# Optimization experiments

Hardware: AMD Instinct MI355X
Metric: run time of the kernel (lower is better)

Reference implementation:

```python
import jax, jax.numpy as jnp
import numpy as np

NUM_GRAPHS = 1024
NODES_PER_GRAPH = 9
EDGES_PER_GRAPH = NODES_PER_GRAPH * (NODES_PER_GRAPH - 1)  # 72, fully connected no self-loops
N = NUM_GRAPHS * NODES_PER_GRAPH
E = NUM_GRAPHS * EDGES_PER_GRAPH
POS_DIM = 64
HID = 256          # gnn_hidden_dim / common_gnn_dim
S1_FEAT = HID      # stage1 feature_dim (after projection)
S1_INT = S1_FEAT + POS_DIM           # 320
S2_FEAT = 2 * HID                    # 512 (two scales concatenated)
S2_OUT = 2 * HID                     # 512
S2_INT = S2_FEAT + POS_DIM           # 576
LN_EPS = 1e-5
SM_EPS = 1e-16  # PyG softmax eps


def _dense(x, w, b):
    return x @ w + b


def _layer_norm(x, g, b):
    mu = jnp.mean(x, axis=-1, keepdims=True)
    var = jnp.mean(jnp.square(x - mu), axis=-1, keepdims=True)
    return (x - mu) * jax.lax.rsqrt(var + LN_EPS) * g + b


def _segment_softmax(logits, idx, n):
    # logits: [E,1]; normalize over edges sharing the same destination node
    m = jax.ops.segment_max(logits, idx, num_segments=n)
    e = jnp.exp(logits - m[idx])
    s = jax.ops.segment_sum(e, idx, num_segments=n)
    return e / (s[idx] + SM_EPS)


def _gnn_layer(x, pos, src, dst, n, p):
    # x: [N, F], pos: [N, P]; edges src->dst (PyG: edge_index[0]=src j, edge_index[1]=dst i)
    ix = jnp.concatenate([x, pos], axis=-1)            # integrated_x [N, F+P]
    ii, ij = ix[dst], ix[src]                          # integrated_x_i / _j per edge
    # pairwise_fn(integrated_x_j, integrated_x_i) -> mlp(cat([integrated_x_i, integrated_x_j]))
    pw_in = jnp.concatenate([ii, ij], axis=-1)         # [E, 2*(F+P)]
    rel = _dense(jax.nn.gelu(_dense(pw_in, p['pw1_w'], p['pw1_b']), approximate=False),
                 p['pw2_w'], p['pw2_b'])               # [E, out]
    att_in = jnp.concatenate([x[dst], x[src], pos[dst], pos[src]], axis=-1)
    logits = _dense(jax.nn.leaky_relu(_dense(att_in, p['att1_w'], p['att1_b']), 0.01),
                    p['att2_w'], p['att2_b'])          # [E, 1]
    attw = _segment_softmax(logits, dst, n)
    aggr = jax.ops.segment_sum(attw * rel, dst, num_segments=n)  # [N, out]
    upd = jax.nn.gelu(_dense(jnp.concatenate([ix, aggr], axis=-1), p['upd_w'], p['upd_b']),
                      approximate=False)
    h = _dense(ix, p['skip_w'], p['skip_b']) + upd
    return _layer_norm(h, p['ln_g'], p['ln_b'])


def _glorot(key, shape):
    fan_in, fan_out = shape[0], shape[1]
    lim = np.sqrt(6.0 / (fan_in + fan_out))
    return jax.random.uniform(key, shape, jnp.float32, -lim, lim)


def setup_inputs() -> dict:
    key = jax.random.key(0)
    ks = iter(jax.random.split(key, 64))

    feat_low = jax.random.normal(next(ks), (N, 512), jnp.float32)
    feat_high = jax.random.normal(next(ks), (N, 1024), jnp.float32)
    batch_indices = jnp.repeat(jnp.arange(NUM_GRAPHS), NODES_PER_GRAPH).astype(jnp.int32)

    # fully connected (no self loop) edges within each 9-node graph
    loc = np.array([(j, i) for i in range(NODES_PER_GRAPH) for j in range(NODES_PER_GRAPH) if i != j],
                   dtype=np.int64)  # (src, dst)
    off = np.repeat(np.arange(NUM_GRAPHS) * NODES_PER_GRAPH, EDGES_PER_GRAPH)
    src = np.tile(loc[:, 0], NUM_GRAPHS) + off
    dst = np.tile(loc[:, 1], NUM_GRAPHS) + off
    edge_index = jnp.asarray(np.stack([src, dst]), dtype=jnp.int32)  # [2, E]

    inp = dict(feat_low=feat_low, feat_high=feat_high,
               batch_indices=batch_indices, edge_index=edge_index)

    inp['pos_table'] = jax.random.normal(next(ks), (NODES_PER_GRAPH, POS_DIM), jnp.float32)
    inp['proj_low_w'] = _glorot(next(ks), (512, HID)); inp['proj_low_b'] = jnp.zeros((HID,), jnp.float32)
    inp['proj_high_w'] = _glorot(next(ks), (1024, HID)); inp['proj_high_b'] = jnp.zeros((HID,), jnp.float32)

    def layer_params(pref, fdim, pdim, out):
        integ = fdim + pdim
        d = {}
        d[pref + 'pw1_w'] = _glorot(next(ks), (2 * integ, out)); d[pref + 'pw1_b'] = jnp.zeros((out,), jnp.float32)
        d[pref + 'pw2_w'] = _glorot(next(ks), (out, out)); d[pref + 'pw2_b'] = jnp.zeros((out,), jnp.float32)
        d[pref + 'att1_w'] = _glorot(next(ks), (2 * fdim + 2 * pdim, out)); d[pref + 'att1_b'] = jnp.zeros((out,), jnp.float32)
        d[pref + 'att2_w'] = _glorot(next(ks), (out, 1)); d[pref + 'att2_b'] = jnp.zeros((1,), jnp.float32)
        d[pref + 'upd_w'] = _glorot(next(ks), (integ + out, out)); d[pref + 'upd_b'] = jnp.zeros((out,), jnp.float32)
        d[pref + 'ln_g'] = jnp.ones((out,), jnp.float32); d[pref + 'ln_b'] = jnp.zeros((out,), jnp.float32)
        d[pref + 'skip_w'] = _glorot(next(ks), (integ, out)); d[pref + 'skip_b'] = jnp.zeros((out,), jnp.float32)
        return d

    inp.update(layer_params('s1_', S1_FEAT, POS_DIM, HID))
    inp.update(layer_params('s2_', S2_FEAT, POS_DIM, S2_OUT))

    inp['cls1_w'] = _glorot(next(ks), (S2_OUT, HID)); inp['cls1_b'] = jnp.zeros((HID,), jnp.float32)
    inp['cls2_w'] = _glorot(next(ks), (HID, 1)); inp['cls2_b'] = jnp.zeros((1,), jnp.float32)
    return inp


def _forward(feat_low, feat_high, pos_table,
             proj_low_w, proj_low_b, proj_high_w, proj_high_b,
             s1, s2, cls1_w, cls1_b, cls2_w, cls2_b,
             batch_indices, edge_index):
    src, dst = edge_index[0], edge_index[1]
    pos_ids = jnp.tile(jnp.arange(NODES_PER_GRAPH), NUM_GRAPHS)
    pos = pos_table[pos_ids]                                  # [N, P]
    h_low = _gnn_layer(_dense(feat_low, proj_low_w, proj_low_b), pos, src, dst, N, s1)
    h_high = _gnn_layer(_dense(feat_high, proj_high_w, proj_high_b), pos, src, dst, N, s1)
    unified = jnp.concatenate([h_low, h_high], axis=-1)       # [N, 512]
    h2 = _gnn_layer(unified, pos, src, dst, N, s2)            # [N, 512]
    pooled = jax.ops.segment_sum(h2, batch_indices, num_segments=NUM_GRAPHS)
    hid = jax.nn.gelu(_dense(pooled, cls1_w, cls1_b), approximate=False)
    return _dense(hid, cls2_w, cls2_b)                        # [G, 1]


S1_KEYS = ['pw1_w', 'pw1_b', 'pw2_w', 'pw2_b', 'att1_w', 'att1_b', 'att2_w', 'att2_b',
           'upd_w', 'upd_b', 'ln_g', 'ln_b', 'skip_w', 'skip_b']


def reference(feat_low, feat_high, batch_indices, edge_index, pos_table,
              proj_low_w, proj_low_b, proj_high_w, proj_high_b,
              s1_pw1_w, s1_pw1_b, s1_pw2_w, s1_pw2_b, s1_att1_w, s1_att1_b,
              s1_att2_w, s1_att2_b, s1_upd_w, s1_upd_b, s1_ln_g, s1_ln_b,
              s1_skip_w, s1_skip_b,
              s2_pw1_w, s2_pw1_b, s2_pw2_w, s2_pw2_b, s2_att1_w, s2_att1_b,
              s2_att2_w, s2_att2_b, s2_upd_w, s2_upd_b, s2_ln_g, s2_ln_b,
              s2_skip_w, s2_skip_b,
              cls1_w, cls1_b, cls2_w, cls2_b):
    s1 = dict(zip(S1_KEYS, [s1_pw1_w, s1_pw1_b, s1_pw2_w, s1_pw2_b, s1_att1_w, s1_att1_b,
                            s1_att2_w, s1_att2_b, s1_upd_w, s1_upd_b, s1_ln_g, s1_ln_b,
                            s1_skip_w, s1_skip_b]))
    s2 = dict(zip(S1_KEYS, [s2_pw1_w, s2_pw1_b, s2_pw2_w, s2_pw2_b, s2_att1_w, s2_att1_b,
                            s2_att2_w, s2_att2_b, s2_upd_w, s2_upd_b, s2_ln_g, s2_ln_b,
                            s2_skip_w, s2_skip_b]))
    return _forward(feat_low, feat_high, pos_table,
                    proj_low_w, proj_low_b, proj_high_w, proj_high_b,
                    s1, s2, cls1_w, cls1_b, cls2_w, cls2_b,
                    batch_indices, edge_index)
```

## Files before the change

### kernel.cpp

```cpp
#include <hip/hip_runtime.h>
#include <math.h>

#define NUM_GRAPHS 1024
#define NPG 9
#define NN 9216
#define NN2 18432
#define POSD 64

typedef __attribute__((ext_vector_type(8))) short bf16x8;
typedef __attribute__((ext_vector_type(4))) float f32x4;

__device__ __forceinline__ float gelu_f(float x) {
    return 0.5f * x * (1.0f + erff(x * 0.70710678118654752f));
}
__device__ __forceinline__ float gelu_fast(float x) {
    float y = 0.7978845608f * x * (1.0f + 0.044715f * x * x);
    float t = __expf(-2.0f * fabsf(y));
    float r = (1.0f - t) / (1.0f + t);
    r = copysignf(r, y);
    return 0.5f * x * (1.0f + r);
}
__device__ __forceinline__ ushort f2b(float v) {
    unsigned u = __float_as_uint(v);
    return (ushort)((u + 0x7fffu + ((u >> 16) & 1u)) >> 16);
}
__device__ __forceinline__ float b2f(ushort u) {
    return __uint_as_float(((unsigned)u) << 16);
}
__device__ __forceinline__ void gload16(const ushort* g, ushort* l) {
    __builtin_amdgcn_global_load_lds((const __attribute__((address_space(1))) void*)g,
                                     (__attribute__((address_space(3))) void*)l, 16, 0, 0);
}

__global__ __launch_bounds__(256, 3) void mgemm(
    const ushort* __restrict__ A, int lda,
    const ushort* __restrict__ Wt, int ldw,
    const float* __restrict__ bias1,
    const float* __restrict__ prow, int ldp,
    float* outF, ushort* outB, int ldo,
    long partStride, int K)
{
    __shared__ ushort sA[3][128 * 32];
    __shared__ ushort sB[3][128 * 32];
    const int wv = threadIdx.x >> 6, lane = threadIdx.x & 63;
    const int rh = wv & 1, ch = wv >> 1;

    const int GX = gridDim.x;
    const int nwg = GX * gridDim.y;
    const int flat = blockIdx.y * GX + blockIdx.x;
    const int swq = nwg >> 3, swr = nwg & 7;
    const int xcd = flat & 7, posi = flat >> 3;
    const int tix = (xcd < swr ? xcd * (swq + 1) : swr * (swq + 1) + (xcd - swr) * swq) + posi;
    const int m0 = (tix / GX) * 128, n0 = (tix % GX) * 128;

    const int koff = blockIdx.z * K;

    f32x4 acc[4][4];
#pragma unroll
    for (int i = 0; i < 4; i++)
#pragma unroll
        for (int j = 0; j < 4; j++) acc[i][j] = (f32x4){0.f, 0.f, 0.f, 0.f};

    const ushort* Ab = A + (size_t)m0 * lda + koff;
    const ushort* Wb = Wt + (size_t)n0 * ldw + koff;
    if (outF) outF += (size_t)blockIdx.z * partStride;

    auto stage = [&](int b, int k0) {
#pragma unroll
        for (int i = 0; i < 2; i++) {
            int c = wv * 2 + i;
            int u = c * 64 + lane;
            int row = u >> 2, p = u & 3;
            int q = (p - (row >> 1)) & 3;
            gload16(Ab + (size_t)row * lda + k0 + q * 8, sA[b] + c * 512);
            gload16(Wb + (size_t)row * ldw + k0 + q * 8, sB[b] + c * 512);
        }
    };

    const int nsteps = K >> 5;
    stage(0, 0);
    stage(1, 32);
    int cur = 0;
    for (int s = 0; s < nsteps; s++) {
        if (s + 1 < nsteps) {
            asm volatile("s_waitcnt vmcnt(4)" ::: "memory");
        } else {
            asm volatile("s_waitcnt vmcnt(0)" ::: "memory");
        }
        __builtin_amdgcn_s_barrier();
        __builtin_amdgcn_sched_barrier(0);
        if (s + 2 < nsteps) {
            int nb = cur + 2; if (nb >= 3) nb -= 3;
            stage(nb, (s + 2) << 5);
        }

        const int qg = lane >> 4;
        bf16x8 af[4], bfr[4];
#pragma unroll
        for (int bi = 0; bi < 4; bi++) {
            int r = rh * 64 + bi * 16 + (lane & 15);
            af[bi] = *(const bf16x8*)(sA[cur] + (r * 4 + ((qg + (r >> 1)) & 3)) * 8);
        }
#pragma unroll
        for (int bj = 0; bj < 4; bj++) {
            int r = ch * 64 + bj * 16 + (lane & 15);
            bfr[bj] = *(const bf16x8*)(sB[cur] + (r * 4 + ((qg + (r >> 1)) & 3)) * 8);
        }
        __builtin_amdgcn_s_setprio(1);
#pragma unroll
        for (int bi = 0; bi < 4; bi++)
#pragma unroll
            for (int bj = 0; bj < 4; bj++)
                acc[bi][bj] = __builtin_amdgcn_mfma_f32_16x16x32_bf16(
                    af[bi], bfr[bj], acc[bi][bj], 0, 0, 0);
        __builtin_amdgcn_s_setprio(0);
        __builtin_amdgcn_sched_barrier(0);
        cur++; if (cur >= 3) cur -= 3;
    }

    float* sP = (float*)sA;
    const bool haveP = (prow != 0);
    if (haveP) {
        __syncthreads();
        for (int i = threadIdx.x; i < 9 * 128; i += 256) {
            int rr = i >> 7, c = i & 127;
            sP[rr * 129 + c] = prow[(size_t)rr * ldp + n0 + c] + bias1[n0 + c];
        }
        __syncthreads();
    }

#pragma unroll
    for (int bi = 0; bi < 4; bi++) {
#pragma unroll
        for (int r = 0; r < 4; r++) {
            int m = m0 + rh * 64 + bi * 16 + (lane >> 4) * 4 + r;
            int r9 = m % 9;
#pragma unroll
            for (int bj = 0; bj < 4; bj++) {
                int nc = ch * 64 + bj * 16 + (lane & 15);
                int n = n0 + nc;
                float v = acc[bi][bj][r];
                if (haveP) v += sP[r9 * 129 + nc];
                if (outF) outF[(size_t)m * ldo + n] = v;
                if (outB) outB[(size_t)m * ldo + n] = f2b(v);
            }
        }
    }
}

struct PJArg {
    const ushort* A[2];
    const ushort* W[2];
    const float*  bias[2];
    ushort*       out[2];
    int lda[2], K[2];
};

__global__ __launch_bounds__(256, 3) void pjgemm(PJArg pa)
{
    __shared__ ushort sA[3][128 * 32];
    __shared__ ushort sB[3][128 * 32];
    const int z = blockIdx.z;
    const ushort* __restrict__ A  = pa.A[z];
    const ushort* __restrict__ Wt = pa.W[z];
    const float*  __restrict__ bias = pa.bias[z];
    ushort* out = pa.out[z];
    const int lda = pa.lda[z], ldw = lda, K = pa.K[z];

    const int wv = threadIdx.x >> 6, lane = threadIdx.x & 63;
    const int rh = wv & 1, ch = wv >> 1;

    const int GX = gridDim.x;
    const int nwg = GX * gridDim.y;
    const int flat = blockIdx.y * GX + blockIdx.x;
    const int swq = nwg >> 3, swr = nwg & 7;
    const int xcd = flat & 7, posi = flat >> 3;
    const int tix = (xcd < swr ? xcd * (swq + 1) : swr * (swq + 1) + (xcd - swr) * swq) + posi;
    const int m0 = (tix / GX) * 128, n0 = (tix % GX) * 128;

    f32x4 acc[4][4];
#pragma unroll
    for (int i = 0; i < 4; i++)
#pragma unroll
        for (int j = 0; j < 4; j++) acc[i][j] = (f32x4){0.f, 0.f, 0.f, 0.f};

    const ushort* Ab = A + (size_t)m0 * lda;
    const ushort* Wb = Wt + (size_t)n0 * ldw;

    auto stage = [&](int b, int k0) {
#pragma unroll
        for (int i = 0; i < 2; i++) {
            int c = wv * 2 + i;
            int u = c * 64 + lane;
            int row = u >> 2, p = u & 3;
            int q = (p - (row >> 1)) & 3;
            gload16(Ab + (size_t)row * lda + k0 + q * 8, sA[b] + c * 512);
            gload16(Wb + (size_t)row * ldw + k0 + q * 8, sB[b] + c * 512);
        }
    };

    const int nsteps = K >> 5;
    stage(0, 0);
    stage(1, 32);
    int cur = 0;
    for (int s = 0; s < nsteps; s++) {
        if (s + 1 < nsteps) {
            asm volatile("s_waitcnt vmcnt(4)" ::: "memory");
        } else {
            asm volatile("s_waitcnt vmcnt(0)" ::: "memory");
        }
        __builtin_amdgcn_s_barrier();
        __builtin_amdgcn_sched_barrier(0);
        if (s + 2 < nsteps) {
            int nb = cur + 2; if (nb >= 3) nb -= 3;
            stage(nb, (s + 2) << 5);
        }

        const int qg = lane >> 4;
        bf16x8 af[4], bfr[4];
#pragma unroll
        for (int bi = 0; bi < 4; bi++) {
            int r = rh * 64 + bi * 16 + (lane & 15);
            af[bi] = *(const bf16x8*)(sA[cur] + (r * 4 + ((qg + (r >> 1)) & 3)) * 8);
        }
#pragma unroll
        for (int bj = 0; bj < 4; bj++) {
            int r = ch * 64 + bj * 16 + (lane & 15);
            bfr[bj] = *(const bf16x8*)(sB[cur] + (r * 4 + ((qg + (r >> 1)) & 3)) * 8);
        }
        __builtin_amdgcn_s_setprio(1);
#pragma unroll
        for (int bi = 0; bi < 4; bi++)
#pragma unroll
            for (int bj = 0; bj < 4; bj++)
                acc[bi][bj] = __builtin_amdgcn_mfma_f32_16x16x32_bf16(
                    af[bi], bfr[bj], acc[bi][bj], 0, 0, 0);
        __builtin_amdgcn_s_setprio(0);
        __builtin_amdgcn_sched_barrier(0);
        cur++; if (cur >= 3) cur -= 3;
    }

    float* sBias = (float*)sA;
    __syncthreads();
    if (threadIdx.x < 128) sBias[threadIdx.x] = bias[n0 + threadIdx.x];
    __syncthreads();

#pragma unroll
    for (int bi = 0; bi < 4; bi++) {
#pragma unroll
        for (int r = 0; r < 4; r++) {
            int m = m0 + rh * 64 + bi * 16 + (lane >> 4) * 4 + r;
#pragma unroll
            for (int bj = 0; bj < 4; bj++) {
                int nc = ch * 64 + bj * 16 + (lane & 15);
                float v = acc[bi][bj][r] + sBias[nc];
                out[(size_t)m * 512 + n0 + nc] = f2b(v);
            }
        }
    }
}

#define NJOBS 16
struct TJobsArg {
    const float* src[NJOBS];
    long dst[NJOBS];
    int K[NJOBS], N[NJOBS], off0[NJOBS], ldo[NJOBS];
};

__global__ __launch_bounds__(256) void tw_kernel(TJobsArg ja, ushort* wbuf)
{
    int j = blockIdx.y;
    int K = ja.K[j], N = ja.N[j];
    int tk = K >> 5, tn = N >> 5;
    int t = blockIdx.x;
    if (t >= tk * tn) return;
    int kt = t % tk, nt = t / tk;
    const float* src = ja.src[j];
    ushort* out = wbuf + ja.dst[j];
    int ldo = ja.ldo[j];
    __shared__ float L[32][33];
    int r = threadIdx.x >> 5, c = threadIdx.x & 31;
#pragma unroll
    for (int rr = 0; rr < 4; rr++) {
        int k = kt * 32 + rr * 8 + r;
        L[rr * 8 + r][c] = src[(size_t)(ja.off0[j] + k) * N + nt * 32 + c];
    }
    __syncthreads();
#pragma unroll
    for (int rr = 0; rr < 4; rr++) {
        int n = nt * 32 + rr * 8 + r;
        out[(size_t)n * ldo + kt * 32 + c] = f2b(L[c][rr * 8 + r]);
    }
}

__global__ __launch_bounds__(256) void edge_kernel(
    const ushort* __restrict__ PB, const float* __restrict__ att2_w,
    ushort* __restrict__ Gout, int ldG, float* __restrict__ S, int O, int cshift)
{
    __shared__ ushort sPB[9 * 1024];
    __shared__ float sAw[512];
    __shared__ float logits[72];
    __shared__ float aw[72];
    const int g = blockIdx.x;
    const int tid = threadIdx.x, lane = tid & 63, wave = tid >> 6;
    const int O2 = O * 2, O5 = O * 5;
    const int tpr = O >> 8;
    const int tcount = 9 * tpr;
    const ushort* gbase = PB + (size_t)g * 9 * O5;

    for (int i = wave; i < tcount; i += 4) {
        int row = i / tpr, co = i - row * tpr;
        gload16(gbase + (size_t)row * O5 + O2 + co * 512 + lane * 8, sPB + i * 512);
    }
    for (int c = tid; c < O; c += 256) sAw[c] = att2_w[c];
    __syncthreads();

    for (int e = wave; e < 72; e += 4) {
        int d = e >> 3, k = e & 7;
        int s = k + (k >= d);
        const ushort* ad = sPB + d * O2;
        const ushort* as = sPB + s * O2 + O;
        float p = 0.f;
        for (int c0 = lane * 4; c0 < O; c0 += 256) {
            ushort4 a4 = *(const ushort4*)(ad + c0);
            ushort4 s4 = *(const ushort4*)(as + c0);
            const ushort* ap = (const ushort*)&a4;
            const ushort* sp = (const ushort*)&s4;
#pragma unroll
            for (int j = 0; j < 4; j++) {
                float v = b2f(ap[j]) + b2f(sp[j]);
                v = v > 0.f ? v : 0.01f * v;
                p += v * sAw[c0 + j];
            }
        }
#pragma unroll
        for (int off = 32; off; off >>= 1) p += __shfl_down(p, off, 64);
        if (lane == 0) logits[e] = p;
    }
    __syncthreads();

    for (int i = wave; i < tcount; i += 4) {
        int row = i / tpr, co = i - row * tpr;
        gload16(gbase + (size_t)row * O5 + co * 512 + lane * 8, sPB + i * 512);
    }

    if (tid < 9) {
        float m = -INFINITY;
#pragma unroll
        for (int k = 0; k < 8; k++) m = fmaxf(m, logits[tid * 8 + k]);
        float s = 0.f, ee[8];
#pragma unroll
        for (int k = 0; k < 8; k++) { ee[k] = expf(logits[tid * 8 + k] - m); s += ee[k]; }
        float inv = 1.0f / (s + 1e-16f);
#pragma unroll
        for (int k = 0; k < 8; k++) aw[tid * 8 + k] = ee[k] * inv;
        S[g * 9 + tid] = s * inv;
    }
    __syncthreads();

    const int nch = O >> 3;
    for (int idx = tid; idx < 9 * nch; idx += 256) {
        int n = idx >> cshift, cc = idx & (nch - 1);
        bf16x8 pdv = *(const bf16x8*)(sPB + n * O2 + cc * 8);
        const ushort* pp = (const ushort*)&pdv;
        float pdf[8];
#pragma unroll
        for (int j = 0; j < 8; j++) pdf[j] = b2f(pp[j]);
        float acc8[8];
#pragma unroll
        for (int j = 0; j < 8; j++) acc8[j] = 0.f;
#pragma unroll
        for (int k = 0; k < 8; k++) {
            int s = k + (k >= n);
            float w = aw[n * 8 + k];
            bf16x8 psv = *(const bf16x8*)(sPB + s * O2 + O + cc * 8);
            const ushort* qp = (const ushort*)&psv;
#pragma unroll
            for (int j = 0; j < 8; j++)
                acc8[j] += w * gelu_fast(pdf[j] + b2f(qp[j]));
        }
        ushort o8[8];
#pragma unroll
        for (int j = 0; j < 8; j++) o8[j] = f2b(acc8[j]);
        *(bf16x8*)(Gout + (size_t)(g * 9 + n) * ldG + cc * 8) = *(const bf16x8*)o8;
    }
}

__global__ __launch_bounds__(256) void ln_kernel(
    const float* __restrict__ P0, const float* __restrict__ P1,
    const float* __restrict__ ub, const float* __restrict__ vb,
    const float* __restrict__ S, const float* __restrict__ posU,
    const ushort* __restrict__ PBs, int ld5,
    const float* __restrict__ gw, const float* __restrict__ bw,
    ushort* outB, int ldoB, int rowsplit, float* outF, int O)
{
    __shared__ float sm[4];
    const int n = blockIdx.x, tid = threadIdx.x;
    const int lane = tid & 63, wid = tid >> 6;
    const float* p0 = P0 + (size_t)n * O;
    const float* p1 = P1 ? P1 + (size_t)n * O : 0;
    const ushort* sr = PBs + (size_t)n * ld5;
    const float* pu = posU + (size_t)(n % 9) * O;
    const float sv = S[n];
    const int cnt = O >> 8;

    float vals[2];
    float sum = 0.f;
#pragma unroll
    for (int i = 0; i < 2; i++) {
        if (i < cnt) {
            int c = tid + 256 * i;
            float t = p0[c] + (p1 ? p1[c] : 0.f) + ub[c] + vb[c] * sv + pu[c];
            vals[i] = gelu_f(t) + b2f(sr[c]);
            sum += vals[i];
        }
    }
#pragma unroll
    for (int off = 32; off; off >>= 1) sum += __shfl_down(sum, off, 64);
    if (lane == 0) sm[wid] = sum;
    __syncthreads();
    const float mu = (sm[0] + sm[1] + sm[2] + sm[3]) / (float)O;
    __syncthreads();

    float var = 0.f;
#pragma unroll
    for (int i = 0; i < 2; i++) {
        if (i < cnt) { float d = vals[i] - mu; var += d * d; }
    }
#pragma unroll
    for (int off = 32; off; off >>= 1) var += __shfl_down(var, off, 64);
    if (lane == 0) sm[wid] = var;
    __syncthreads();
    const float rstd = rsqrtf((sm[0] + sm[1] + sm[2] + sm[3]) / (float)O + 1e-5f);

    int orow = n, coloff = 0;
    if (n >= rowsplit) { orow = n - rowsplit; coloff = 256; }
#pragma unroll
    for (int i = 0; i < 2; i++) {
        if (i < cnt) {
            int c = tid + 256 * i;
            float v = (vals[i] - mu) * rstd * gw[c] + bw[c];
            if (outB) outB[(size_t)orow * ldoB + coloff + c] = f2b(v);
            if (outF) outF[(size_t)n * O + c] = v;
        }
    }
}

__global__ void prep_kernel(
    const float* __restrict__ pw1_b1, const float* __restrict__ att1_b1, const float* __restrict__ skip_b1,
    const float* __restrict__ pw1_b2, const float* __restrict__ att1_b2, const float* __restrict__ skip_b2,
    const float* __restrict__ pos_table,
    const float* __restrict__ s1_pw1, const float* __restrict__ s1_att, const float* __restrict__ s1_skp,
    const float* __restrict__ s2_pw1, const float* __restrict__ s2_att, const float* __restrict__ s2_skp,
    const float* __restrict__ pw2_b1, const float* __restrict__ upd_w1,
    const float* __restrict__ pw2_b2, const float* __restrict__ upd_w2,
    const float* __restrict__ pw2_w1, const float* __restrict__ pw2_w2,
    const float* __restrict__ feat_low, const float* __restrict__ feat_high,
    float* biasC1, float* biasC2,
    float* posPB1, float* posPB2, float* posU1, float* posU2,
    float* vb1, float* vb2, ushort* pw2f1, ushort* pw2f2, ushort* featB)
{
    int i = blockIdx.x * 256 + threadIdx.x;
    if (i < 1280) {
        float v;
        if (i < 256) v = pw1_b1[i];
        else if (i < 512) v = 0.f;
        else if (i < 768) v = att1_b1[i - 512];
        else if (i < 1024) v = 0.f;
        else v = skip_b1[i - 1024];
        biasC1[i] = v;
        return;
    }
    i -= 1280;
    if (i < 2560) {
        float v;
        if (i < 512) v = pw1_b2[i];
        else if (i < 1024) v = 0.f;
        else if (i < 1536) v = att1_b2[i - 1024];
        else if (i < 2048) v = 0.f;
        else v = skip_b2[i - 2048];
        biasC2[i] = v;
        return;
    }
    i -= 2560;
    if (i < 9 * 1280) {
        int r = i / 1280, n = i - r * 1280;
        int sec = n >> 8, c = n & 255;
        const float* src; int row0;
        if (sec == 0) { src = s1_pw1; row0 = 256; }
        else if (sec == 1) { src = s1_pw1; row0 = 576; }
        else if (sec == 2) { src = s1_att; row0 = 512; }
        else if (sec == 3) { src = s1_att; row0 = 576; }
        else { src = s1_skp; row0 = 256; }
        float a = 0.f;
        for (int k = 0; k < 64; k++) a += pos_table[r * 64 + k] * src[(size_t)(row0 + k) * 256 + c];
        posPB1[i] = a;
        return;
    }
    i -= 9 * 1280;
    if (i < 9 * 2560) {
        int r = i / 2560, n = i - r * 2560;
        int sec = n >> 9, c = n & 511;
        const float* src; int row0;
        if (sec == 0) { src = s2_pw1; row0 = 512; }
        else if (sec == 1) { src = s2_pw1; row0 = 1088; }
        else if (sec == 2) { src = s2_att; row0 = 1024; }
        else if (sec == 3) { src = s2_att; row0 = 1088; }
        else { src = s2_skp; row0 = 512; }
        float a = 0.f;
        for (int k = 0; k < 64; k++) a += pos_table[r * 64 + k] * src[(size_t)(row0 + k) * 512 + c];
        posPB2[i] = a;
        return;
    }
    i -= 9 * 2560;
    if (i < 9 * 256) {
        int r = i >> 8, c = i & 255;
        float a = 0.f;
        for (int k = 0; k < 64; k++) a += pos_table[r * 64 + k] * upd_w1[(size_t)(256 + k) * 256 + c];
        posU1[i] = a;
        return;
    }
    i -= 9 * 256;
    if (i < 9 * 512) {
        int r = i >> 9, c = i & 511;
        float a = 0.f;
        for (int k = 0; k < 64; k++) a += pos_table[r * 64 + k] * upd_w2[(size_t)(512 + k) * 512 + c];
        posU2[i] = a;
        return;
    }
    i -= 9 * 512;
    if (i < 256) {
        float a = 0.f;
        for (int j = 0; j < 256; j++) a += pw2_b1[j] * upd_w1[(size_t)(320 + j) * 256 + i];
        vb1[i] = a;
        return;
    }
    i -= 256;
    if (i < 512) {
        float a = 0.f;
        for (int j = 0; j < 512; j++) a += pw2_b2[j] * upd_w2[(size_t)(576 + j) * 512 + i];
        vb2[i] = a;
        return;
    }
    i -= 512;
    if (i < 256 * 256) { pw2f1[i] = f2b(pw2_w1[i]); return; }
    i -= 256 * 256;
    if (i < 512 * 512) { pw2f2[i] = f2b(pw2_w2[i]); return; }
    i -= 512 * 512;
    if (i < NN * 512 / 4) {
        float4 v = ((const float4*)feat_low)[i];
        ushort4 o;
        o.x = f2b(v.x); o.y = f2b(v.y); o.z = f2b(v.z); o.w = f2b(v.w);
        ((ushort4*)featB)[i] = o;
        return;
    }
    i -= NN * 512 / 4;
    if (i < NN * 1024 / 4) {
        float4 v = ((const float4*)feat_high)[i];
        ushort4 o;
        o.x = f2b(v.x); o.y = f2b(v.y); o.z = f2b(v.z); o.w = f2b(v.w);
        ((ushort4*)(featB + (size_t)NN * 512))[i] = o;
    }
}

__global__ __launch_bounds__(256) void head_kernel(
    const float* __restrict__ h2,
    const float* __restrict__ cls1_w, const float* __restrict__ cls1_b,
    const float* __restrict__ cls2_w, const float* __restrict__ cls2_b,
    float* __restrict__ out)
{
    __shared__ float pooled[4][512];
    __shared__ float hid[4][256];
    const int b = blockIdx.x, tid = threadIdx.x;

    for (int idx = tid; idx < 4 * 512; idx += 256) {
        int gi = idx >> 9, c = idx & 511;
        const float* base = h2 + (size_t)((b * 4 + gi) * 9) * 512 + c;
        float s = 0.f;
#pragma unroll
        for (int k = 0; k < NPG; k++) s += base[(size_t)k * 512];
        pooled[gi][c] = s;
    }
    __syncthreads();

    {
        float acc[4] = {0.f, 0.f, 0.f, 0.f};
        for (int c = 0; c < 512; c++) {
            float w = cls1_w[(size_t)c * 256 + tid];
#pragma unroll
            for (int gi = 0; gi < 4; gi++) acc[gi] += pooled[gi][c] * w;
        }
        float bb = cls1_b[tid];
#pragma unroll
        for (int gi = 0; gi < 4; gi++) hid[gi][tid] = gelu_f(acc[gi] + bb);
    }
    __syncthreads();

    {
        int gi = tid >> 6, lane = tid & 63;
        float p = 0.f;
#pragma unroll
        for (int i = 0; i < 4; i++) p += hid[gi][lane + 64 * i] * cls2_w[lane + 64 * i];
#pragma unroll
        for (int off = 32; off; off >>= 1) p += __shfl_down(p, off, 64);
        if (lane == 0) out[b * 4 + gi] = p + cls2_b[0];
    }
}

static inline void mg(hipStream_t st, int M, int N, int K,
                      const ushort* A, int lda, const ushort* Wt, int ldw,
                      const float* bias1, const float* prow, int ldp,
                      float* outF, ushort* outB, int ldo,
                      int nz, long partStride)
{
    dim3 grid(N / 128, M / 128, nz);
    mgemm<<<grid, dim3(256), 0, st>>>(A, lda, Wt, ldw, bias1, prow, ldp,
                                      outF, outB, ldo, partStride, K);
}

extern "C" void kernel_launch(void* const* d_in, const int* in_sizes, int n_in,
                              void* d_out, int out_size, void* d_ws, size_t ws_size,
                              hipStream_t stream)
{
    (void)in_sizes; (void)n_in; (void)out_size; (void)ws_size;
    const float* feat_low   = (const float*)d_in[0];
    const float* feat_high  = (const float*)d_in[1];
    const float* pos_table  = (const float*)d_in[4];
    const float* proj_low_w  = (const float*)d_in[5];
    const float* proj_low_b  = (const float*)d_in[6];
    const float* proj_high_w = (const float*)d_in[7];
    const float* proj_high_b = (const float*)d_in[8];
    const float* cls1_w = (const float*)d_in[37];
    const float* cls1_b = (const float*)d_in[38];
    const float* cls2_w = (const float*)d_in[39];
    const float* cls2_b = (const float*)d_in[40];
    float* out = (float*)d_out;

    const float* s1_pw1 = (const float*)d_in[9];
    const float* s1_att = (const float*)d_in[13];
    const float* s1_upd = (const float*)d_in[17];
    const float* s1_skp = (const float*)d_in[21];
    const float* s2_pw1 = (const float*)d_in[23];
    const float* s2_att = (const float*)d_in[27];
    const float* s2_upd = (const float*)d_in[31];
    const float* s2_skp = (const float*)d_in[35];

    const float* att2_w1 = (const float*)d_in[15];
    const float* upd_b1  = (const float*)d_in[18];
    const float* ln_g1   = (const float*)d_in[19];
    const float* ln_b1   = (const float*)d_in[20];
    const float* att2_w2 = (const float*)d_in[29];
    const float* upd_b2  = (const float*)d_in[32];
    const float* ln_g2   = (const float*)d_in[33];
    const float* ln_b2   = (const float*)d_in[34];

    char* base = (char*)d_ws;
    size_t cur = 0;
    auto alloc = [&](size_t bytes) { void* p = base + cur; cur += (bytes + 255) & ~(size_t)255; return p; };
    void*   PBreg = alloc((size_t)NN * 2560 * 2);
    ushort* PB    = (ushort*)PBreg;
    ushort* featB = (ushort*)PBreg;
    void*   IX1reg = alloc((size_t)NN2 * 512 * 2);
    ushort* ixa1  = (ushort*)IX1reg;
    float*  h2    = (float*)IX1reg;
    ushort* ixa2  = (ushort*)alloc((size_t)NN * 1024 * 2);
    float*  PT    = (float*)alloc((size_t)4 * NN * 256 * 4);
    float*  S     = (float*)alloc((size_t)NN2 * 4);
    float*  biasC1 = (float*)alloc(1280 * 4);
    float*  biasC2 = (float*)alloc(2560 * 4);
    float*  posPB1 = (float*)alloc(9 * 1280 * 4);
    float*  posPB2 = (float*)alloc(9 * 2560 * 4);
    float*  posU1  = (float*)alloc(9 * 256 * 4);
    float*  posU2  = (float*)alloc(9 * 512 * 4);
    float*  vb1   = (float*)alloc(256 * 4);
    float*  vb2   = (float*)alloc(512 * 4);
    ushort* wbuf  = (ushort*)alloc((size_t)3400000 * 2);

    TJobsArg ja;
    long woff[16];
    {
        struct J { const float* s; int K, N, off0, ldo; long sz; };
        J js[NJOBS] = {
            {proj_low_w,  512, 256, 0, 512, 512L * 256},
            {proj_high_w, 1024, 256, 0, 1024, 1024L * 256},
            {s1_pw1, 256, 256, 0, 256, 256L * 256},
            {s1_pw1, 256, 256, 320, 256, 256L * 256},
            {s1_att, 256, 256, 0, 256, 256L * 256},
            {s1_att, 256, 256, 256, 256, 256L * 256},
            {s1_skp, 256, 256, 0, 256, 256L * 256},
            {s1_upd, 256, 256, 0, 512, 512L * 256},
            {s1_upd, 256, 256, 320, 256, 256L * 256},
            {s2_pw1, 512, 512, 0, 512, 512L * 512},
            {s2_pw1, 512, 512, 576, 512, 512L * 512},
            {s2_att, 512, 512, 0, 512, 512L * 512},
            {s2_att, 512, 512, 512, 512, 512L * 512},
            {s2_skp, 512, 512, 0, 512, 512L * 512},
            {s2_upd, 512, 512, 0, 1024, 1024L * 512},
            {s2_upd, 512, 512, 576, 512, 512L * 512},
        };
        long off = 0;
        for (int i = 0; i < NJOBS; i++) {
            ja.src[i] = js[i].s; ja.K[i] = js[i].K; ja.N[i] = js[i].N;
            ja.off0[i] = js[i].off0; ja.ldo[i] = js[i].ldo;
            ja.dst[i] = off; woff[i] = off;
            off += js[i].sz;
        }
    }
    long pw2off1 = woff[15] + 512L * 512;
    long pw2off2 = pw2off1 + 256L * 256;
    tw_kernel<<<dim3(256, NJOBS), dim3(256), 0, stream>>>(ja, wbuf);

    ushort* wBig5_1 = wbuf + woff[2];
    ushort* updW1   = wbuf + woff[7];
    ushort* updbT1  = wbuf + woff[8];
    ushort* wBig5_2 = wbuf + woff[9];
    ushort* updW2   = wbuf + woff[14];
    ushort* updbT2  = wbuf + woff[15];
    ushort* pw2f1   = wbuf + pw2off1;
    ushort* pw2f2   = wbuf + pw2off2;

    {
        long tot = 1280 + 2560 + 9 * 1280 + 9 * 2560 + 9 * 256 + 9 * 512
                 + 256 + 512 + 256 * 256 + 512 * 512
                 + (long)NN * 512 / 4 + (long)NN * 1024 / 4;
        prep_kernel<<<dim3((unsigned)((tot + 255) / 256)), dim3(256), 0, stream>>>(
            (const float*)d_in[10], (const float*)d_in[14], (const float*)d_in[22],
            (const float*)d_in[24], (const float*)d_in[28], (const float*)d_in[36],
            pos_table,
            s1_pw1, s1_att, s1_skp, s2_pw1, s2_att, s2_skp,
            (const float*)d_in[12], s1_upd, (const float*)d_in[26], s2_upd,
            (const float*)d_in[11], (const float*)d_in[25],
            feat_low, feat_high,
            biasC1, biasC2, posPB1, posPB2, posU1, posU2, vb1, vb2, pw2f1, pw2f2, featB);
    }

    mg(stream, 256, 256, 256, updbT1, 256, pw2f1, 256, 0, 0, 0, 0, updW1 + 256, 512, 1, 0);
    mg(stream, 512, 512, 512, updbT2, 512, pw2f2, 512, 0, 0, 0, 0, updW2 + 512, 1024, 1, 0);

    {
        PJArg pa;
        pa.A[0] = featB;                      pa.lda[0] = 512;  pa.K[0] = 512;
        pa.A[1] = featB + (size_t)NN * 512;   pa.lda[1] = 1024; pa.K[1] = 1024;
        pa.W[0] = wbuf + woff[0];
        pa.W[1] = wbuf + woff[1];
        pa.bias[0] = proj_low_b;
        pa.bias[1] = proj_high_b;
        pa.out[0] = ixa1;
        pa.out[1] = ixa1 + (size_t)NN * 512;
        pjgemm<<<dim3(2, NN / 128, 2), dim3(256), 0, stream>>>(pa);
    }

    mg(stream, NN2, 1280, 256, ixa1, 512, wBig5_1, 256, biasC1, posPB1, 1280, 0, PB, 1280, 1, 0);
    edge_kernel<<<dim3(2 * NUM_GRAPHS), dim3(256), 0, stream>>>(
        PB, att2_w1, ixa1 + 256, 512, S, 256, 5);
    mg(stream, NN2, 256, 512, ixa1, 512, updW1, 512, 0, 0, 0, PT, 0, 256, 1, 0);
    ln_kernel<<<dim3(NN2), dim3(256), 0, stream>>>(
        PT, 0, upd_b1, vb1, S, posU1,
        PB + 4 * 256, 1280, ln_g1, ln_b1, ixa2, 1024, NN, 0, 256);

    mg(stream, NN, 2560, 512, ixa2, 1024, wBig5_2, 512, biasC2, posPB2, 2560, 0, PB, 2560, 1, 0);
    edge_kernel<<<dim3(NUM_GRAPHS), dim3(256), 0, stream>>>(
        PB, att2_w2, ixa2 + 512, 1024, S, 512, 6);
    mg(stream, NN, 512, 1024, ixa2, 1024, updW2, 1024, 0, 0, 0, PT, 0, 512, 1, 0);
    ln_kernel<<<dim3(NN), dim3(256), 0, stream>>>(
        PT, 0, upd_b2, vb2, S, posU2,
        PB + 4 * 512, 2560, ln_g2, ln_b2, 0, 0, 1 << 30, h2, 512);

    head_kernel<<<dim3(NUM_GRAPHS / 4), dim3(256), 0, stream>>>(h2, cls1_w, cls1_b, cls2_w, cls2_b, out);
}
```

Before: 552.5 us.

## Stage GEMM epilogue through LDS, write bf16 update outputs, one-wave-per-row LayerNorm

The GEMM epilogue now packs bf16 results into a padded LDS tile and writes full rows with 16-byte stores, where it used to do scattered per-element global stores. The fp32 output path is removed. The update GEMMs now emit bf16 into a smaller PT buffer, which halves the traffic they write and the LayerNorm then reads. The LayerNorm kernel is reworked so each wave handles one row with vector loads and xor-shuffle reductions, with no shared memory or block barriers. This trades some precision in the pre-activation values for less memory traffic and fewer launches of small blocks.

```diff
diff --git a/kernel.cpp b/kernel.cpp
--- a/kernel.cpp
+++ b/kernel.cpp
@@ -37,11 +37,9 @@
     const ushort* __restrict__ Wt, int ldw,
     const float* __restrict__ bias1,
     const float* __restrict__ prow, int ldp,
-    float* outF, ushort* outB, int ldo,
-    long partStride, int K)
+    ushort* __restrict__ outB, int ldo, int K)
 {
-    __shared__ ushort sA[3][128 * 32];
-    __shared__ ushort sB[3][128 * 32];
+    __shared__ ushort smem[24576];
     const int wv = threadIdx.x >> 6, lane = threadIdx.x & 63;
     const int rh = wv & 1, ch = wv >> 1;
 
@@ -53,27 +51,26 @@
     const int tix = (xcd < swr ? xcd * (swq + 1) : swr * (swq + 1) + (xcd - swr) * swq) + posi;
     const int m0 = (tix / GX) * 128, n0 = (tix % GX) * 128;
 
-    const int koff = blockIdx.z * K;
-
     f32x4 acc[4][4];
 #pragma unroll
     for (int i = 0; i < 4; i++)
 #pragma unroll
         for (int j = 0; j < 4; j++) acc[i][j] = (f32x4){0.f, 0.f, 0.f, 0.f};
 
-    const ushort* Ab = A + (size_t)m0 * lda + koff;
-    const ushort* Wb = Wt + (size_t)n0 * ldw + koff;
-    if (outF) outF += (size_t)blockIdx.z * partStride;
+    const ushort* Ab = A + (size_t)m0 * lda;
+    const ushort* Wb = Wt + (size_t)n0 * ldw;
 
     auto stage = [&](int b, int k0) {
+        ushort* sA = smem + b * 4096;
+        ushort* sB = smem + 12288 + b * 4096;
 #pragma unroll
         for (int i = 0; i < 2; i++) {
             int c = wv * 2 + i;
             int u = c * 64 + lane;
             int row = u >> 2, p = u & 3;
             int q = (p - (row >> 1)) & 3;
-            gload16(Ab + (size_t)row * lda + k0 + q * 8, sA[b] + c * 512);
-            gload16(Wb + (size_t)row * ldw + k0 + q * 8, sB[b] + c * 512);
+            gload16(Ab + (size_t)row * lda + k0 + q * 8, sA + c * 512);
+            gload16(Wb + (size_t)row * ldw + k0 + q * 8, sB + c * 512);
         }
     };
 
@@ -94,17 +91,19 @@
             stage(nb, (s + 2) << 5);
         }
 
+        const ushort* sA = smem + cur * 4096;
+        const ushort* sB = smem + 12288 + cur * 4096;
         const int qg = lane >> 4;
         bf16x8 af[4], bfr[4];
 #pragma unroll
         for (int bi = 0; bi < 4; bi++) {
             int r = rh * 64 + bi * 16 + (lane & 15);
-            af[bi] = *(const bf16x8*)(sA[cur] + (r * 4 + ((qg + (r >> 1)) & 3)) * 8);
+            af[bi] = *(const bf16x8*)(sA + (r * 4 + ((qg + (r >> 1)) & 3)) * 8);
         }
 #pragma unroll
         for (int bj = 0; bj < 4; bj++) {
             int r = ch * 64 + bj * 16 + (lane & 15);
-            bfr[bj] = *(const bf16x8*)(sB[cur] + (r * 4 + ((qg + (r >> 1)) & 3)) * 8);
+            bfr[bj] = *(const bf16x8*)(sB + (r * 4 + ((qg + (r >> 1)) & 3)) * 8);
         }
         __builtin_amdgcn_s_setprio(1);
 #pragma unroll
@@ -118,33 +117,40 @@
         cur++; if (cur >= 3) cur -= 3;
     }
 
-    float* sP = (float*)sA;
+    __syncthreads();
+    float* sP = (float*)smem;
     const bool haveP = (prow != 0);
     if (haveP) {
-        __syncthreads();
         for (int i = threadIdx.x; i < 9 * 128; i += 256) {
             int rr = i >> 7, c = i & 127;
             sP[rr * 129 + c] = prow[(size_t)rr * ldp + n0 + c] + bias1[n0 + c];
         }
         __syncthreads();
     }
-
+    ushort* T = smem + 4096;
 #pragma unroll
     for (int bi = 0; bi < 4; bi++) {
 #pragma unroll
         for (int r = 0; r < 4; r++) {
-            int m = m0 + rh * 64 + bi * 16 + (lane >> 4) * 4 + r;
-            int r9 = m % 9;
+            int row = rh * 64 + bi * 16 + (lane >> 4) * 4 + r;
+            int r9 = (m0 + row) % 9;
 #pragma unroll
             for (int bj = 0; bj < 4; bj++) {
-                int nc = ch * 64 + bj * 16 + (lane & 15);
-                int n = n0 + nc;
+                int col = ch * 64 + bj * 16 + (lane & 15);
                 float v = acc[bi][bj][r];
-                if (haveP) v += sP[r9 * 129 + nc];
-                if (outF) outF[(size_t)m * ldo + n] = v;
-                if (outB) outB[(size_t)m * ldo + n] = f2b(v);
+                if (haveP) v += sP[r9 * 129 + col];
+                T[row * 136 + col] = f2b(v);
             }
         }
+    }
+    __syncthreads();
+    {
+        int row = threadIdx.x >> 1, half = threadIdx.x & 1;
+        const ushort* src = T + row * 136 + half * 64;
+        ushort* dst = outB + (size_t)(m0 + row) * ldo + n0 + half * 64;
+#pragma unroll
+        for (int j = 0; j < 8; j++)
+            *(bf16x8*)(dst + j * 8) = *(const bf16x8*)(src + j * 8);
     }
 }
 
@@ -387,61 +393,90 @@
 }
 
 __global__ __launch_bounds__(256) void ln_kernel(
-    const float* __restrict__ P0, const float* __restrict__ P1,
+    const ushort* __restrict__ P0,
     const float* __restrict__ ub, const float* __restrict__ vb,
     const float* __restrict__ S, const float* __restrict__ posU,
     const ushort* __restrict__ PBs, int ld5,
     const float* __restrict__ gw, const float* __restrict__ bw,
     ushort* outB, int ldoB, int rowsplit, float* outF, int O)
 {
-    __shared__ float sm[4];
-    const int n = blockIdx.x, tid = threadIdx.x;
-    const int lane = tid & 63, wid = tid >> 6;
-    const float* p0 = P0 + (size_t)n * O;
-    const float* p1 = P1 ? P1 + (size_t)n * O : 0;
+    const int wid = threadIdx.x >> 6, lane = threadIdx.x & 63;
+    const int n = blockIdx.x * 4 + wid;
+    const float sv = S[n];
+    const ushort* p0 = P0 + (size_t)n * O;
     const ushort* sr = PBs + (size_t)n * ld5;
     const float* pu = posU + (size_t)(n % 9) * O;
-    const float sv = S[n];
-    const int cnt = O >> 8;
-
-    float vals[2];
+    const int q = O >> 6;
+    const int c0 = lane * q;
+
+    float vals[8];
     float sum = 0.f;
-#pragma unroll
-    for (int i = 0; i < 2; i++) {
-        if (i < cnt) {
-            int c = tid + 256 * i;
-            float t = p0[c] + (p1 ? p1[c] : 0.f) + ub[c] + vb[c] * sv + pu[c];
-            vals[i] = gelu_f(t) + b2f(sr[c]);
-            sum += vals[i];
-        }
-    }
-#pragma unroll
-    for (int off = 32; off; off >>= 1) sum += __shfl_down(sum, off, 64);
-    if (lane == 0) sm[wid] = sum;
-    __syncthreads();
-    const float mu = (sm[0] + sm[1] + sm[2] + sm[3]) / (float)O;
-    __syncthreads();
-
+    if (O == 256) {
+        ushort4 pv = *(const ushort4*)(p0 + c0);
+        ushort4 sk = *(const ushort4*)(sr + c0);
+        float4 uu = *(const float4*)(ub + c0);
+        float4 vv = *(const float4*)(vb + c0);
+        float4 gg = *(const float4*)(pu + c0);
+        const ushort tp[4] = {pv.x, pv.y, pv.z, pv.w};
+        const ushort ts[4] = {sk.x, sk.y, sk.z, sk.w};
+        const float tu[4] = {uu.x, uu.y, uu.z, uu.w};
+        const float tv[4] = {vv.x, vv.y, vv.z, vv.w};
+        const float tg[4] = {gg.x, gg.y, gg.z, gg.w};
+#pragma unroll
+        for (int j = 0; j < 4; j++) {
+            float t = b2f(tp[j]) + tu[j] + tv[j] * sv + tg[j];
+            vals[j] = gelu_f(t) + b2f(ts[j]);
+            sum += vals[j];
+        }
+    } else {
+        bf16x8 pv = *(const bf16x8*)(p0 + c0);
+        bf16x8 sk = *(const bf16x8*)(sr + c0);
+        const ushort* tp = (const ushort*)&pv;
+        const ushort* ts = (const ushort*)&sk;
+        float4 u0 = *(const float4*)(ub + c0), u1 = *(const float4*)(ub + c0 + 4);
+        float4 v0 = *(const float4*)(vb + c0), v1 = *(const float4*)(vb + c0 + 4);
+        float4 g0 = *(const float4*)(pu + c0), g1 = *(const float4*)(pu + c0 + 4);
+        const float tu[8] = {u0.x,u0.y,u0.z,u0.w, u1.x,u1.y,u1.z,u1.w};
+        const float tv[8] = {v0.x,v0.y,v0.z,v0.w, v1.x,v1.y,v1.z,v1.w};
+        const float tg[8] = {g0.x,g0.y,g0.z,g0.w, g1.x,g1.y,g1.z,g1.w};
+#pragma unroll
+        for (int j = 0; j < 8; j++) {
+            float t = b2f(tp[j]) + tu[j] + tv[j] * sv + tg[j];
+            vals[j] = gelu_f(t) + b2f(ts[j]);
+            sum += vals[j];
+        }
+    }
+
+#pragma unroll
+    for (int off = 32; off; off >>= 1) sum += __shfl_xor(sum, off, 64);
+    const float mu = sum / (float)O;
     float var = 0.f;
 #pragma unroll
-    for (int i = 0; i < 2; i++) {
-        if (i < cnt) { float d = vals[i] - mu; var += d * d; }
-    }
-#pragma unroll
-    for (int off = 32; off; off >>= 1) var += __shfl_down(var, off, 64);
-    if (lane == 0) sm[wid] = var;
-    __syncthreads();
-    const float rstd = rsqrtf((sm[0] + sm[1] + sm[2] + sm[3]) / (float)O + 1e-5f);
+    for (int j = 0; j < 8; j++) {
+        if (j < q) { float d = vals[j] - mu; var += d * d; }
+    }
+#pragma unroll
+    for (int off = 32; off; off >>= 1) var += __shfl_xor(var, off, 64);
+    const float rstd = rsqrtf(var / (float)O + 1e-5f);
 
     int orow = n, coloff = 0;
     if (n >= rowsplit) { orow = n - rowsplit; coloff = 256; }
-#pragma unroll
-    for (int i = 0; i < 2; i++) {
-        if (i < cnt) {
-            int c = tid + 256 * i;
-            float v = (vals[i] - mu) * rstd * gw[c] + bw[c];
-            if (outB) outB[(size_t)orow * ldoB + coloff + c] = f2b(v);
-            if (outF) outF[(size_t)n * O + c] = v;
+
+    if (outB) {
+        ushort o[8];
+#pragma unroll
+        for (int j = 0; j < 8; j++) {
+            if (j < q) o[j] = f2b((vals[j] - mu) * rstd * gw[c0 + j] + bw[c0 + j]);
+        }
+        ushort* dst = outB + (size_t)orow * ldoB + coloff + c0;
+        if (q == 4) *(ushort4*)dst = *(const ushort4*)o;
+        else        *(bf16x8*)dst = *(const bf16x8*)o;
+    }
+    if (outF) {
+        float* dst = outF + (size_t)n * O + c0;
+#pragma unroll
+        for (int j = 0; j < 8; j++) {
+            if (j < q) dst[j] = (vals[j] - mu) * rstd * gw[c0 + j] + bw[c0 + j];
         }
     }
 }
@@ -610,12 +645,11 @@
 static inline void mg(hipStream_t st, int M, int N, int K,
                       const ushort* A, int lda, const ushort* Wt, int ldw,
                       const float* bias1, const float* prow, int ldp,
-                      float* outF, ushort* outB, int ldo,
-                      int nz, long partStride)
+                      ushort* outB, int ldo)
 {
-    dim3 grid(N / 128, M / 128, nz);
+    dim3 grid(N / 128, M / 128);
     mgemm<<<grid, dim3(256), 0, st>>>(A, lda, Wt, ldw, bias1, prow, ldp,
-                                      outF, outB, ldo, partStride, K);
+                                      outB, ldo, K);
 }
 
 extern "C" void kernel_launch(void* const* d_in, const int* in_sizes, int n_in,
@@ -664,7 +698,7 @@
     ushort* ixa1  = (ushort*)IX1reg;
     float*  h2    = (float*)IX1reg;
     ushort* ixa2  = (ushort*)alloc((size_t)NN * 1024 * 2);
-    float*  PT    = (float*)alloc((size_t)4 * NN * 256 * 4);
+    ushort* PT    = (ushort*)alloc((size_t)NN2 * 512 * 2);
     float*  S     = (float*)alloc((size_t)NN2 * 4);
     float*  biasC1 = (float*)alloc(1280 * 4);
     float*  biasC2 = (float*)alloc(2560 * 4);
@@ -734,8 +768,8 @@
             biasC1, biasC2, posPB1, posPB2, posU1, posU2, vb1, vb2, pw2f1, pw2f2, featB);
     }
 
-    mg(stream, 256, 256, 256, updbT1, 256, pw2f1, 256, 0, 0, 0, 0, updW1 + 256, 512, 1, 0);
-    mg(stream, 512, 512, 512, updbT2, 512, pw2f2, 512, 0, 0, 0, 0, updW2 + 512, 1024, 1, 0);
+    mg(stream, 256, 256, 256, updbT1, 256, pw2f1, 256, 0, 0, 0, updW1 + 256, 512);
+    mg(stream, 512, 512, 512, updbT2, 512, pw2f2, 512, 0, 0, 0, updW2 + 512, 1024);
 
     {
         PJArg pa;
@@ -750,20 +784,20 @@
         pjgemm<<<dim3(2, NN / 128, 2), dim3(256), 0, stream>>>(pa);
     }
 
-    mg(stream, NN2, 1280, 256, ixa1, 512, wBig5_1, 256, biasC1, posPB1, 1280, 0, PB, 1280, 1, 0);
+    mg(stream, NN2, 1280, 256, ixa1, 512, wBig5_1, 256, biasC1, posPB1, 1280, PB, 1280);
     edge_kernel<<<dim3(2 * NUM_GRAPHS), dim3(256), 0, stream>>>(
         PB, att2_w1, ixa1 + 256, 512, S, 256, 5);
-    mg(stream, NN2, 256, 512, ixa1, 512, updW1, 512, 0, 0, 0, PT, 0, 256, 1, 0);
-    ln_kernel<<<dim3(NN2), dim3(256), 0, stream>>>(
-        PT, 0, upd_b1, vb1, S, posU1,
+    mg(stream, NN2, 256, 512, ixa1, 512, updW1, 512, 0, 0, 0, PT, 256);
+    ln_kernel<<<dim3(NN2 / 4), dim3(256), 0, stream>>>(
+        PT, upd_b1, vb1, S, posU1,
         PB + 4 * 256, 1280, ln_g1, ln_b1, ixa2, 1024, NN, 0, 256);
 
-    mg(stream, NN, 2560, 512, ixa2, 1024, wBig5_2, 512, biasC2, posPB2, 2560, 0, PB, 2560, 1, 0);
+    mg(stream, NN, 2560, 512, ixa2, 1024, wBig5_2, 512, biasC2, posPB2, 2560, PB, 2560);
     edge_kernel<<<dim3(NUM_GRAPHS), dim3(256), 0, stream>>>(
         PB, att2_w2, ixa2 + 512, 1024, S, 512, 6);
-    mg(stream, NN, 512, 1024, ixa2, 1024, updW2, 1024, 0, 0, 0, PT, 0, 512, 1, 0);
-    ln_kernel<<<dim3(NN), dim3(256), 0, stream>>>(
-        PT, 0, upd_b2, vb2, S, posU2,
+    mg(stream, NN, 512, 1024, ixa2, 1024, updW2, 1024, 0, 0, 0, PT, 512);
+    ln_kernel<<<dim3(NN / 4), dim3(256), 0, stream>>>(
+        PT, upd_b2, vb2, S, posU2,
         PB + 4 * 512, 2560, ln_g2, ln_b2, 0, 0, 1 << 30, h2, 512);
 
     head_kernel<<<dim3(NUM_GRAPHS / 4), dim3(256), 0, stream>>>(h2, cls1_w, cls1_b, cls2_w, cls2_b, out);
```

Result: faster. 539.4 us (-2.4%).
